# Performance work log

Measured on AMD Instinct MI355X. Metric: run time of the kernel, lower is better.

## Reference

```python
import jax, jax.numpy as jnp
import numpy as np

N, C, T = 65536, 1000, 2.0

def setup_inputs() -> dict:
    key = jax.random.key(0)
    k1, k2, k3, k4 = jax.random.split(key, 4)
    return {
        "outputs1": jax.random.normal(k1, (N, C), dtype=jnp.float32),
        "outputs2": jax.random.normal(k2, (N, C), dtype=jnp.float32),
        "mimic": jax.random.normal(k3, (N, C), dtype=jnp.float32),
        "targets": jax.random.randint(k4, (N,), 0, C, dtype=jnp.int64),
        "n_test": N,
    }

def _margin(x, targets):
    # top-2 per row; margin = top1 - top2 if target logit equals the max, else 0
    top2, _ = jax.lax.top_k(x, 2)                       # [N, 2]
    tgt_logit = jnp.take_along_axis(x, targets[:, None], axis=1)[:, 0]  # [N]
    return jnp.where(tgt_logit == top2[:, 0], top2[:, 0] - top2[:, 1], 0.0)

def reference(outputs1, outputs2, mimic, targets, n_test):
    d1 = _margin(outputs1, targets)
    d2 = _margin(outputs2, targets)
    m = _margin(mimic, targets)
    preds = jnp.stack([d1, d2, m], axis=1)              # [N, 3]
    out_threshold = jax.nn.softmax(preds / T, axis=1)   # softmax over the 3 margins
    max_preds = jnp.maximum(outputs1.max(), outputs2.max())
    return (max_preds, out_threshold)
```

## Files before the change

kernel.cpp:

```cpp
#include <hip/hip_runtime.h>
#include <math.h>

#define NEG_INF (-__builtin_inff())

__device__ __forceinline__ void top2_update(float v, float& m1, float& m2) {
    float nm1 = fmaxf(m1, v);
    m2 = fmaxf(m2, fminf(m1, v));
    m1 = nm1;
}

__device__ __forceinline__ void upd4(float4 v, float& m1, float& m2) {
    top2_update(v.x, m1, m2); top2_update(v.y, m1, m2);
    top2_update(v.z, m1, m2); top2_update(v.w, m1, m2);
}

__device__ __forceinline__ void top2_merge(float o1, float o2, float& m1, float& m2) {
    float hi = fmaxf(m1, o1);
    float lo = fminf(m1, o1);
    m2 = fmaxf(lo, fmaxf(m2, o2));
    m1 = hi;
}

__device__ __forceinline__ unsigned int enc_float(float f) {
    unsigned int b = __float_as_uint(f);
    return (b & 0x80000000u) ? ~b : (b | 0x80000000u);
}

__global__ __launch_bounds__(256) void margin_softmax_kernel(
    const float* __restrict__ out1,
    const float* __restrict__ out2,
    const float* __restrict__ mim,
    const int*   __restrict__ targets,
    float*       __restrict__ d_out,
    int N)
{
    const int C = 1000;
    const int lane          = threadIdx.x & 63;
    const int wave_in_blk   = threadIdx.x >> 6;
    const int waves_per_blk = blockDim.x >> 6;
    const int gwave  = blockIdx.x * waves_per_blk + wave_in_blk;
    const int nwaves = gridDim.x * waves_per_blk;

    float lane_run = NEG_INF;

    for (int row = gwave; row < N; row += nwaves) {
        const size_t base = (size_t)row * (size_t)C;
        const float4* p1 = (const float4*)(out1 + base);
        const float4* p2 = (const float4*)(out2 + base);
        const float4* p3 = (const float4*)(mim  + base);

        float4 A0 = p1[lane], A1 = p1[lane + 64], A2 = p1[lane + 128];
        float4 B0 = p2[lane], B1 = p2[lane + 64], B2 = p2[lane + 128];
        float4 M0 = p3[lane], M1 = p3[lane + 64], M2 = p3[lane + 128];
        float4 A3 = make_float4(NEG_INF, NEG_INF, NEG_INF, NEG_INF);
        float4 B3 = A3, M3 = A3;
        if (lane < 58) {
            A3 = p1[lane + 192];
            B3 = p2[lane + 192];
            M3 = p3[lane + 192];
        }

        float a1 = NEG_INF, a2 = NEG_INF;
        float b1 = NEG_INF, b2 = NEG_INF;
        float c1 = NEG_INF, c2 = NEG_INF;

        upd4(A0, a1, a2); upd4(A1, a1, a2); upd4(A2, a1, a2); upd4(A3, a1, a2);
        upd4(B0, b1, b2); upd4(B1, b1, b2); upd4(B2, b1, b2); upd4(B3, b1, b2);
        upd4(M0, c1, c2); upd4(M1, c1, c2); upd4(M2, c1, c2); upd4(M3, c1, c2);

        #pragma unroll
        for (int off = 32; off >= 1; off >>= 1) {
            float o1, o2;
            o1 = __shfl_xor(a1, off); o2 = __shfl_xor(a2, off); top2_merge(o1, o2, a1, a2);
            o1 = __shfl_xor(b1, off); o2 = __shfl_xor(b2, off); top2_merge(o1, o2, b1, b2);
            o1 = __shfl_xor(c1, off); o2 = __shfl_xor(c2, off); top2_merge(o1, o2, c1, c2);
        }

        lane_run = fmaxf(lane_run, fmaxf(a1, b1));

        if (lane == 0) {
            int tgt = targets[row];
            float t1 = out1[base + tgt];
            float t2 = out2[base + tgt];
            float t3 = mim [base + tgt];
            float d1 = (t1 == a1) ? (a1 - a2) : 0.0f;
            float d2 = (t2 == b1) ? (b1 - b2) : 0.0f;
            float d3 = (t3 == c1) ? (c1 - c2) : 0.0f;
            float x1 = d1 * 0.5f, x2 = d2 * 0.5f, x3 = d3 * 0.5f;
            float mx = fmaxf(x1, fmaxf(x2, x3));
            float e1 = expf(x1 - mx), e2 = expf(x2 - mx), e3 = expf(x3 - mx);
            float inv = 1.0f / (e1 + e2 + e3);
            float* o = d_out + 1 + (size_t)row * 3;
            o[0] = e1 * inv;
            o[1] = e2 * inv;
            o[2] = e3 * inv;
        }
    }

    #pragma unroll
    for (int off = 32; off >= 1; off >>= 1)
        lane_run = fmaxf(lane_run, __shfl_xor(lane_run, off));

    __shared__ float smax[8];
    if (lane == 0) smax[wave_in_blk] = lane_run;
    __syncthreads();
    if (threadIdx.x == 0) {
        float m = smax[0];
        for (int i = 1; i < waves_per_blk; i++) m = fmaxf(m, smax[i]);
        atomicMax((unsigned int*)d_out, enc_float(m));
    }
}

__global__ void finalize_max_kernel(float* d_out) {
    unsigned int u = ((unsigned int*)d_out)[0];
    unsigned int b = (u & 0x80000000u) ? (u ^ 0x80000000u) : ~u;
    d_out[0] = __uint_as_float(b);
}

extern "C" void kernel_launch(void* const* d_in, const int* in_sizes, int n_in,
                              void* d_out, int out_size, void* d_ws, size_t ws_size,
                              hipStream_t stream) {
    const float* out1    = (const float*)d_in[0];
    const float* out2    = (const float*)d_in[1];
    const float* mim     = (const float*)d_in[2];
    const int*   targets = (const int*)  d_in[3];

    const int N = in_sizes[3];

    (void)hipMemsetAsync(d_out, 0, sizeof(unsigned int), stream);

    margin_softmax_kernel<<<2048, 256, 0, stream>>>(
        out1, out2, mim, targets, (float*)d_out, N);

    finalize_max_kernel<<<1, 1, 0, stream>>>((float*)d_out);
}
```

Before: 649.2 us.

## Prefetch next row into registers and read target logit from loaded data

```diff
diff --git a/kernel.cpp b/kernel.cpp
--- a/kernel.cpp
+++ b/kernel.cpp
@@ -26,7 +26,21 @@
     return (b & 0x80000000u) ? ~b : (b | 0x80000000u);
 }
 
-__global__ __launch_bounds__(256) void margin_softmax_kernel(
+__device__ __forceinline__ float sel4(float4 v, int e) {
+    float xy = (e & 1) ? v.y : v.x;
+    float zw = (e & 1) ? v.w : v.z;
+    return (e & 2) ? zw : xy;
+}
+
+__device__ __forceinline__ float selg(float4 a0, float4 a1, float4 a2, float4 a3,
+                                      int g, int e) {
+    float s0 = sel4(a0, e), s1 = sel4(a1, e), s2 = sel4(a2, e), s3 = sel4(a3, e);
+    float lo = (g & 1) ? s1 : s0;
+    float hi = (g & 1) ? s3 : s2;
+    return (g & 2) ? hi : lo;
+}
+
+__global__ __launch_bounds__(256, 4) void margin_softmax_kernel(
     const float* __restrict__ out1,
     const float* __restrict__ out2,
     const float* __restrict__ mim,
@@ -34,39 +48,59 @@
     float*       __restrict__ d_out,
     int N)
 {
-    const int C = 1000;
     const int lane          = threadIdx.x & 63;
     const int wave_in_blk   = threadIdx.x >> 6;
     const int waves_per_blk = blockDim.x >> 6;
     const int gwave  = blockIdx.x * waves_per_blk + wave_in_blk;
     const int nwaves = gridDim.x * waves_per_blk;
 
+    const float4 pad = make_float4(NEG_INF, NEG_INF, NEG_INF, NEG_INF);
+
     float lane_run = NEG_INF;
 
-    for (int row = gwave; row < N; row += nwaves) {
-        const size_t base = (size_t)row * (size_t)C;
-        const float4* p1 = (const float4*)(out1 + base);
-        const float4* p2 = (const float4*)(out2 + base);
-        const float4* p3 = (const float4*)(mim  + base);
+    float4 A0, A1, A2, A3, B0, B1, B2, B3, M0, M1, M2, M3;
+    int tgt = 0;
 
-        float4 A0 = p1[lane], A1 = p1[lane + 64], A2 = p1[lane + 128];
-        float4 B0 = p2[lane], B1 = p2[lane + 64], B2 = p2[lane + 128];
-        float4 M0 = p3[lane], M1 = p3[lane + 64], M2 = p3[lane + 128];
-        float4 A3 = make_float4(NEG_INF, NEG_INF, NEG_INF, NEG_INF);
-        float4 B3 = A3, M3 = A3;
-        if (lane < 58) {
-            A3 = p1[lane + 192];
-            B3 = p2[lane + 192];
-            M3 = p3[lane + 192];
-        }
+#define ISSUE_ROW(r)                                                        \
+    do {                                                                    \
+        const size_t base_ = (size_t)(r) * 1000u;                           \
+        const float4* q1 = (const float4*)(out1 + base_);                   \
+        const float4* q2 = (const float4*)(out2 + base_);                   \
+        const float4* q3 = (const float4*)(mim  + base_);                   \
+        tgt = targets[r];                                                   \
+        A0 = q1[lane];       B0 = q2[lane];       M0 = q3[lane];            \
+        A1 = q1[lane + 64];  B1 = q2[lane + 64];  M1 = q3[lane + 64];       \
+        A2 = q1[lane + 128]; B2 = q2[lane + 128]; M2 = q3[lane + 128];      \
+        A3 = pad; B3 = pad; M3 = pad;                                       \
+        if (lane < 58) {                   \
+            A3 = q1[lane + 192]; B3 = q2[lane + 192]; M3 = q3[lane + 192];  \
+        }                                                                   \
+    } while (0)
+
+    int row = gwave;
+    if (row < N) ISSUE_ROW(row);
+
+    for (; row < N; row += nwaves) {
+        const int nrow = row + nwaves;
 
         float a1 = NEG_INF, a2 = NEG_INF;
         float b1 = NEG_INF, b2 = NEG_INF;
         float c1 = NEG_INF, c2 = NEG_INF;
 
-        upd4(A0, a1, a2); upd4(A1, a1, a2); upd4(A2, a1, a2); upd4(A3, a1, a2);
-        upd4(B0, b1, b2); upd4(B1, b1, b2); upd4(B2, b1, b2); upd4(B3, b1, b2);
-        upd4(M0, c1, c2); upd4(M1, c1, c2); upd4(M2, c1, c2); upd4(M3, c1, c2);
+        upd4(A0, a1, a2); upd4(B0, b1, b2); upd4(M0, c1, c2);
+        upd4(A1, a1, a2); upd4(B1, b1, b2); upd4(M1, c1, c2);
+        upd4(A2, a1, a2); upd4(B2, b1, b2); upd4(M2, c1, c2);
+        upd4(A3, a1, a2); upd4(B3, b1, b2); upd4(M3, c1, c2);
+
+        const int q  = tgt >> 2;
+        const int lt = q & 63;
+        const int g  = q >> 6;
+        const int e  = tgt & 3;
+        float tv1 = selg(A0, A1, A2, A3, g, e);
+        float tv2 = selg(B0, B1, B2, B3, g, e);
+        float tv3 = selg(M0, M1, M2, M3, g, e);
+
+        if (nrow < N) ISSUE_ROW(nrow);
 
         #pragma unroll
         for (int off = 32; off >= 1; off >>= 1) {
@@ -78,14 +112,10 @@
 
         lane_run = fmaxf(lane_run, fmaxf(a1, b1));
 
-        if (lane == 0) {
-            int tgt = targets[row];
-            float t1 = out1[base + tgt];
-            float t2 = out2[base + tgt];
-            float t3 = mim [base + tgt];
-            float d1 = (t1 == a1) ? (a1 - a2) : 0.0f;
-            float d2 = (t2 == b1) ? (b1 - b2) : 0.0f;
-            float d3 = (t3 == c1) ? (c1 - c2) : 0.0f;
+        if (lane == lt) {
+            float d1 = (tv1 == a1) ? (a1 - a2) : 0.0f;
+            float d2 = (tv2 == b1) ? (b1 - b2) : 0.0f;
+            float d3 = (tv3 == c1) ? (c1 - c2) : 0.0f;
             float x1 = d1 * 0.5f, x2 = d2 * 0.5f, x3 = d3 * 0.5f;
             float mx = fmaxf(x1, fmaxf(x2, x3));
             float e1 = expf(x1 - mx), e2 = expf(x2 - mx), e3 = expf(x3 - mx);
@@ -96,10 +126,7 @@
             o[2] = e3 * inv;
         }
     }
-
-    #pragma unroll
-    for (int off = 32; off >= 1; off >>= 1)
-        lane_run = fmaxf(lane_run, __shfl_xor(lane_run, off));
+#undef ISSUE_ROW
 
     __shared__ float smax[8];
     if (lane == 0) smax[wave_in_blk] = lane_run;
```

Result: slower. 676.5 us (+4.2%).
